# Kernel tuning notes

Hardware: AMD Instinct MI355X
Metric: run time of the kernel (lower is better)

## Reference

```python
import jax, jax.numpy as jnp
import numpy as np

B, T, D, H = 64, 512, 512, 1024


def setup_inputs() -> dict:
    key = jax.random.key(0)
    k_x, k_m, k_wi, k_wh = jax.random.split(key, 4)
    x = jax.random.normal(k_x, (B, T, D), dtype=jnp.float32)
    mask = jax.random.randint(k_m, (B, T), 0, 2, dtype=jnp.int32)
    # LSTMCell params: xavier_uniform for W_ih, orthogonal for W_hh, zero biases
    lim = float(np.sqrt(6.0 / (4 * H + D)))
    W_ih = jax.random.uniform(k_wi, (4 * H, D), dtype=jnp.float32, minval=-lim, maxval=lim)
    A = jax.random.normal(k_wh, (4 * H, H), dtype=jnp.float32)
    Q, _ = jnp.linalg.qr(A.T)  # (H, 4H) columns orthonormal -> rows of W_hh orthogonal-ish per torch init
    W_hh = Q.T.astype(jnp.float32)
    W_hh = jnp.concatenate([W_hh] * ((4 * H) // W_hh.shape[0]), axis=0)[: 4 * H]
    b_ih = jnp.zeros((4 * H,), dtype=jnp.float32)
    b_hh = jnp.zeros((4 * H,), dtype=jnp.float32)
    h0 = jnp.zeros((1, H), dtype=jnp.float32)
    c0 = jnp.zeros((1, H), dtype=jnp.float32)
    return {"x": x, "mask": mask, "W_ih": W_ih, "W_hh": W_hh,
            "b_ih": b_ih, "b_hh": b_hh, "h0": h0, "c0": c0}


def reference(x, mask, W_ih, W_hh, b_ih, b_hh, h0, c0):
    Bn, Tn, _ = x.shape
    Hn = h0.shape[1]
    # Precompute input projection for all timesteps: (B, T, 4H)
    xg = jnp.einsum('btd,gd->btg', x, W_ih) + b_ih + b_hh

    def step(carry, inp):
        h, c = carry
        xg_t, m_t = inp  # (B, 4H), (B,)
        gates = xg_t + h @ W_hh.T  # (B, 4H)
        i, f, g, o = jnp.split(gates, 4, axis=-1)  # torch LSTMCell gate order i,f,g,o
        i = jax.nn.sigmoid(i)
        f = jax.nn.sigmoid(f)
        g = jnp.tanh(g)
        o = jax.nn.sigmoid(o)
        c_new = f * c + i * g
        h_new = o * jnp.tanh(c_new)
        keep = (m_t != 0)[:, None]
        h2 = jnp.where(keep, h_new, h)
        c2 = jnp.where(keep, c_new, c)
        return (h2, c2), h2

    h_init = jnp.broadcast_to(h0, (Bn, Hn))
    c_init = jnp.broadcast_to(c0, (Bn, Hn))
    xs = (jnp.swapaxes(xg, 0, 1), mask.T)  # time-major for scan
    (_, _), hs = jax.lax.scan(step, (h_init, c_init), xs)
    return jnp.swapaxes(hs, 0, 1)  # (B, T, H)
```

## Files before the change

### kernel.cpp

```cpp
#include <hip/hip_runtime.h>

#define B_   64
#define T_   512
#define D_   512
#define H_   1024
#define G4   4096
#define KTOT 1536
#define KC_N 48
#define AP   1544

typedef float f32x4 __attribute__((ext_vector_type(4)));
typedef short s16x8 __attribute__((ext_vector_type(8)));

__device__ __forceinline__ unsigned short f2bf(float f) {
    unsigned int u = __float_as_uint(f);
    u = (u + 0x7fffu + ((u >> 16) & 1u)) >> 16;
    return (unsigned short)u;
}
__device__ __forceinline__ float bf2f(unsigned short h) {
    return __uint_as_float(((unsigned int)h) << 16);
}
__device__ __forceinline__ float sigm(float x) { return 1.f / (1.f + __expf(-x)); }
__device__ __forceinline__ float tanh_f(float x) { return 1.f - 2.f / (__expf(2.f * x) + 1.f); }

__global__ __launch_bounds__(256) void pack_w(const float* __restrict__ W_ih,
                                              const float* __restrict__ W_hh,
                                              unsigned short* __restrict__ Wpk) {
    int tid = blockIdx.x * 256 + threadIdx.x;
    int j    = tid & 7;
    int lane = (tid >> 3) & 63;
    int rest = tid >> 9;
    int kc = rest % KC_N;
    int c  = rest / KC_N;
    int npk = c * 16 + (lane & 15);
    int jh = npk >> 2, g = npk & 3;
    int row = g * H_ + jh;
    int k = kc * 32 + (lane >> 4) * 8 + j;
    float v = (k < D_) ? W_ih[row * D_ + k] : W_hh[row * H_ + (k - D_)];
    Wpk[tid] = f2bf(v);
}

__global__ __launch_bounds__(256) void init_state(const float* __restrict__ h0,
                                                  const float* __restrict__ c0,
                                                  const float* __restrict__ b_ih,
                                                  const float* __restrict__ b_hh,
                                                  unsigned short* __restrict__ h_a,
                                                  float* __restrict__ c_cur,
                                                  float* __restrict__ bias_p) {
    int tid = blockIdx.x * 256 + threadIdx.x;
    int j = tid & (H_ - 1);
    h_a[tid]  = f2bf(h0[j]);
    c_cur[tid] = c0[j];
    if (tid < G4) {
        int jh = tid >> 2, g = tid & 3;
        bias_p[tid] = b_ih[g * H_ + jh] + b_hh[g * H_ + jh];
    }
}

__global__ __launch_bounds__(256) void lstm_step(
    const float* __restrict__ x, const int* __restrict__ mask,
    const unsigned short* __restrict__ Wpk, const float* __restrict__ bias_p,
    const unsigned short* __restrict__ h_in, unsigned short* __restrict__ h_out,
    float* __restrict__ c_cur, float* __restrict__ out, int t)
{
    __shared__ unsigned short At[16 * AP];
    __shared__ float Dl[16][66];

    const int tid = threadIdx.x;
    const int b0 = blockIdx.y * 16;
    const int bx = blockIdx.x;

    #pragma unroll
    for (int i = 0; i < 8; ++i) {
        int e = i * 256 + tid;
        int r = e >> 7, c4 = e & 127;
        float4 v = *reinterpret_cast<const float4*>(x + ((b0 + r) * T_ + t) * D_ + c4 * 4);
        unsigned int lo = ((unsigned int)f2bf(v.y) << 16) | f2bf(v.x);
        unsigned int hi = ((unsigned int)f2bf(v.w) << 16) | f2bf(v.z);
        *reinterpret_cast<uint2*>(&At[r * AP + c4 * 4]) = make_uint2(lo, hi);
    }
    #pragma unroll
    for (int i = 0; i < 8; ++i) {
        int e = i * 256 + tid;
        int r = e >> 7, c8 = e & 127;
        uint4 v = *reinterpret_cast<const uint4*>(h_in + (b0 + r) * H_ + c8 * 8);
        *reinterpret_cast<uint4*>(&At[r * AP + D_ + c8 * 8]) = v;
    }
    __syncthreads();

    const int w = tid >> 6, l = tid & 63;
    const int quad = l >> 4, l15 = l & 15;
    const int cgrp = bx * 4 + w;

    f32x4 acc = {0.f, 0.f, 0.f, 0.f};
    const unsigned short* atp = &At[l15 * AP + quad * 8];
    const unsigned short* bp  = Wpk + ((size_t)(cgrp * KC_N) * 64 + l) * 8;
    #pragma unroll 4
    for (int kc = 0; kc < KC_N; ++kc) {
        s16x8 af = *reinterpret_cast<const s16x8*>(atp + kc * 32);
        s16x8 bf = *reinterpret_cast<const s16x8*>(bp + kc * 64 * 8);
        acc = __builtin_amdgcn_mfma_f32_16x16x32_bf16(af, bf, acc, 0, 0, 0);
    }
    #pragma unroll
    for (int r = 0; r < 4; ++r)
        Dl[quad * 4 + r][w * 16 + l15] = acc[r];
    __syncthreads();

    const int b = tid >> 4, u = tid & 15;
    const int jh = bx * 16 + u;
    float4 bias = *reinterpret_cast<const float4*>(bias_p + bx * 64 + u * 4);
    float gi = sigm (Dl[b][u * 4 + 0] + bias.x);
    float gf = sigm (Dl[b][u * 4 + 1] + bias.y);
    float gg = tanh_f(Dl[b][u * 4 + 2] + bias.z);
    float go = sigm (Dl[b][u * 4 + 3] + bias.w);

    const int sidx = (b0 + b) * H_ + jh;
    float c_old = c_cur[sidx];
    float h_old = bf2f(At[b * AP + D_ + jh]);
    float c_new = gf * c_old + gi * gg;
    float h_new = go * tanh_f(c_new);
    int m = mask[(b0 + b) * T_ + t];
    float h2 = m ? h_new : h_old;
    float c2 = m ? c_new : c_old;
    c_cur[sidx] = c2;
    h_out[sidx] = f2bf(h2);
    out[((size_t)(b0 + b) * T_ + t) * H_ + jh] = h2;
}

extern "C" void kernel_launch(void* const* d_in, const int* in_sizes, int n_in,
                              void* d_out, int out_size, void* d_ws, size_t ws_size,
                              hipStream_t stream)
{
    const float* x    = (const float*)d_in[0];
    const int*   mask = (const int*)d_in[1];
    const float* W_ih = (const float*)d_in[2];
    const float* W_hh = (const float*)d_in[3];
    const float* b_ih = (const float*)d_in[4];
    const float* b_hh = (const float*)d_in[5];
    const float* h0   = (const float*)d_in[6];
    const float* c0   = (const float*)d_in[7];
    float* out = (float*)d_out;

    char* wsb = (char*)d_ws;
    unsigned short* Wpk    = (unsigned short*)(wsb);
    float*          bias_p = (float*)(wsb + 12582912);
    unsigned short* h_a    = (unsigned short*)(wsb + 12599296);
    unsigned short* h_b    = (unsigned short*)(wsb + 12730368);
    float*          c_cur  = (float*)(wsb + 12861440);

    pack_w<<<24576, 256, 0, stream>>>(W_ih, W_hh, Wpk);
    init_state<<<256, 256, 0, stream>>>(h0, c0, b_ih, b_hh, h_a, c_cur, bias_p);

    dim3 grid(64, 4);
    for (int t = 0; t < T_; ++t) {
        const unsigned short* hin = (t & 1) ? h_b : h_a;
        unsigned short*      hout = (t & 1) ? h_a : h_b;
        lstm_step<<<grid, 256, 0, stream>>>(x, mask, Wpk, bias_p, hin, hout, c_cur, out, t);
    }
}
```

Before: 3.451 ms.

## Replace per-timestep launches with persistent LSTM kernel using grid barriers

```diff
diff --git a/kernel.cpp b/kernel.cpp
--- a/kernel.cpp
+++ b/kernel.cpp
@@ -5,9 +5,8 @@
 #define D_   512
 #define H_   1024
 #define G4   4096
-#define KTOT 1536
 #define KC_N 48
-#define AP   1544
+#define NBLK_HALF 128
 
 typedef float f32x4 __attribute__((ext_vector_type(4)));
 typedef short s16x8 __attribute__((ext_vector_type(8)));
@@ -17,11 +16,17 @@
     u = (u + 0x7fffu + ((u >> 16) & 1u)) >> 16;
     return (unsigned short)u;
 }
-__device__ __forceinline__ float bf2f(unsigned short h) {
-    return __uint_as_float(((unsigned int)h) << 16);
-}
 __device__ __forceinline__ float sigm(float x) { return 1.f / (1.f + __expf(-x)); }
 __device__ __forceinline__ float tanh_f(float x) { return 1.f - 2.f / (__expf(2.f * x) + 1.f); }
+
+__device__ __forceinline__ s16x8 cvt8(float4 a, float4 b) {
+    union { s16x8 v; unsigned int u[4]; } r;
+    asm("v_cvt_pk_bf16_f32 %0, %1, %2" : "=v"(r.u[0]) : "v"(a.x), "v"(a.y));
+    asm("v_cvt_pk_bf16_f32 %0, %1, %2" : "=v"(r.u[1]) : "v"(a.z), "v"(a.w));
+    asm("v_cvt_pk_bf16_f32 %0, %1, %2" : "=v"(r.u[2]) : "v"(b.x), "v"(b.y));
+    asm("v_cvt_pk_bf16_f32 %0, %1, %2" : "=v"(r.u[3]) : "v"(b.z), "v"(b.w));
+    return r.v;
+}
 
 __global__ __launch_bounds__(256) void pack_w(const float* __restrict__ W_ih,
                                               const float* __restrict__ W_hh,
@@ -40,91 +45,140 @@
     Wpk[tid] = f2bf(v);
 }
 
-__global__ __launch_bounds__(256) void init_state(const float* __restrict__ h0,
-                                                  const float* __restrict__ c0,
-                                                  const float* __restrict__ b_ih,
-                                                  const float* __restrict__ b_hh,
-                                                  unsigned short* __restrict__ h_a,
-                                                  float* __restrict__ c_cur,
-                                                  float* __restrict__ bias_p) {
+__global__ __launch_bounds__(256) void init_state2(
+    const float* __restrict__ h0, const float* __restrict__ b_ih,
+    const float* __restrict__ b_hh, unsigned short* __restrict__ hbuf,
+    float* __restrict__ bias_p, unsigned int* __restrict__ bar)
+{
     int tid = blockIdx.x * 256 + threadIdx.x;
     int j = tid & (H_ - 1);
-    h_a[tid]  = f2bf(h0[j]);
-    c_cur[tid] = c0[j];
+    hbuf[tid] = f2bf(h0[j]);
     if (tid < G4) {
         int jh = tid >> 2, g = tid & 3;
         bias_p[tid] = b_ih[g * H_ + jh] + b_hh[g * H_ + jh];
     }
-}
-
-__global__ __launch_bounds__(256) void lstm_step(
+    if (tid < 64) bar[tid] = 0u;
+}
+
+__global__ __launch_bounds__(512, 2) void lstm_persist(
     const float* __restrict__ x, const int* __restrict__ mask,
     const unsigned short* __restrict__ Wpk, const float* __restrict__ bias_p,
-    const unsigned short* __restrict__ h_in, unsigned short* __restrict__ h_out,
-    float* __restrict__ c_cur, float* __restrict__ out, int t)
+    const float* __restrict__ h0, const float* __restrict__ c0,
+    unsigned short* __restrict__ hbuf, float* __restrict__ out,
+    unsigned int* __restrict__ bar)
 {
-    __shared__ unsigned short At[16 * AP];
-    __shared__ float Dl[16][66];
-
     const int tid = threadIdx.x;
-    const int b0 = blockIdx.y * 16;
-    const int bx = blockIdx.x;
-
-    #pragma unroll
-    for (int i = 0; i < 8; ++i) {
-        int e = i * 256 + tid;
-        int r = e >> 7, c4 = e & 127;
-        float4 v = *reinterpret_cast<const float4*>(x + ((b0 + r) * T_ + t) * D_ + c4 * 4);
-        unsigned int lo = ((unsigned int)f2bf(v.y) << 16) | f2bf(v.x);
-        unsigned int hi = ((unsigned int)f2bf(v.w) << 16) | f2bf(v.z);
-        *reinterpret_cast<uint2*>(&At[r * AP + c4 * 4]) = make_uint2(lo, hi);
-    }
-    #pragma unroll
-    for (int i = 0; i < 8; ++i) {
-        int e = i * 256 + tid;
-        int r = e >> 7, c8 = e & 127;
-        uint4 v = *reinterpret_cast<const uint4*>(h_in + (b0 + r) * H_ + c8 * 8);
-        *reinterpret_cast<uint4*>(&At[r * AP + D_ + c8 * 8]) = v;
-    }
-    __syncthreads();
+    const int bid = blockIdx.x;
+    const int cg  = bid >> 1;
+    const int mh  = bid & 1;
+    const int b0g = mh << 5;
 
     const int w = tid >> 6, l = tid & 63;
     const int quad = l >> 4, l15 = l & 15;
-    const int cgrp = bx * 4 + w;
-
-    f32x4 acc = {0.f, 0.f, 0.f, 0.f};
-    const unsigned short* atp = &At[l15 * AP + quad * 8];
-    const unsigned short* bp  = Wpk + ((size_t)(cgrp * KC_N) * 64 + l) * 8;
-    #pragma unroll 4
-    for (int kc = 0; kc < KC_N; ++kc) {
-        s16x8 af = *reinterpret_cast<const s16x8*>(atp + kc * 32);
-        s16x8 bf = *reinterpret_cast<const s16x8*>(bp + kc * 64 * 8);
-        acc = __builtin_amdgcn_mfma_f32_16x16x32_bf16(af, bf, acc, 0, 0, 0);
-    }
+    const int mi = w >> 2;
+    const int ks = w & 3;
+    const int arow = b0g + mi * 16 + l15;
+
+    __shared__ float Dls[4][32][36];
+
+    s16x8 Bf0[12], Bf1[12];
     #pragma unroll
-    for (int r = 0; r < 4; ++r)
-        Dl[quad * 4 + r][w * 16 + l15] = acc[r];
-    __syncthreads();
-
-    const int b = tid >> 4, u = tid & 15;
-    const int jh = bx * 16 + u;
-    float4 bias = *reinterpret_cast<const float4*>(bias_p + bx * 64 + u * 4);
-    float gi = sigm (Dl[b][u * 4 + 0] + bias.x);
-    float gf = sigm (Dl[b][u * 4 + 1] + bias.y);
-    float gg = tanh_f(Dl[b][u * 4 + 2] + bias.z);
-    float go = sigm (Dl[b][u * 4 + 3] + bias.w);
-
-    const int sidx = (b0 + b) * H_ + jh;
-    float c_old = c_cur[sidx];
-    float h_old = bf2f(At[b * AP + D_ + jh]);
-    float c_new = gf * c_old + gi * gg;
-    float h_new = go * tanh_f(c_new);
-    int m = mask[(b0 + b) * T_ + t];
-    float h2 = m ? h_new : h_old;
-    float c2 = m ? c_new : c_old;
-    c_cur[sidx] = c2;
-    h_out[sidx] = f2bf(h2);
-    out[((size_t)(b0 + b) * T_ + t) * H_ + jh] = h2;
+    for (int i = 0; i < 12; ++i) {
+        int kc = ks * 12 + i;
+        Bf0[i] = *reinterpret_cast<const s16x8*>(Wpk + (size_t)(((cg * 2 + 0) * KC_N + kc) * 64 + l) * 8);
+        Bf1[i] = *reinterpret_cast<const s16x8*>(Wpk + (size_t)(((cg * 2 + 1) * KC_N + kc) * 64 + l) * 8);
+    }
+
+    const int b_l = tid >> 3, u = tid & 7;
+    const int brow = b0g + b_l;
+    const int jcol = cg * 8 + u;
+    float c_reg = 0.f, h_reg = 0.f;
+    float4 bias = make_float4(0.f, 0.f, 0.f, 0.f);
+    if (tid < 256) {
+        c_reg = c0[jcol];
+        h_reg = h0[jcol];
+        bias = *reinterpret_cast<const float4*>(bias_p + cg * 32 + u * 4);
+    }
+
+    unsigned int* cnt = bar + mh * 32;
+
+    #pragma unroll 1
+    for (int t = 0; t < T_; ++t) {
+        const unsigned short* hin  = hbuf + (size_t)(t & 1) * (B_ * H_);
+        unsigned short*       hout = hbuf + (size_t)((t + 1) & 1) * (B_ * H_);
+
+        f32x4 a0 = {0.f, 0.f, 0.f, 0.f}, a1 = {0.f, 0.f, 0.f, 0.f};
+        const float* xrow = x + ((size_t)arow * T_ + t) * D_;
+        #pragma unroll
+        for (int i = 0; i < 12; ++i) {
+            int kc = ks * 12 + i;
+            s16x8 af;
+            if (kc < 16) {
+                const float* xp = xrow + kc * 32 + quad * 8;
+                float4 v0 = *reinterpret_cast<const float4*>(xp);
+                float4 v1 = *reinterpret_cast<const float4*>(xp + 4);
+                af = cvt8(v0, v1);
+            } else {
+                const unsigned int* hp = reinterpret_cast<const unsigned int*>(
+                    hin + (size_t)arow * H_ + (kc - 16) * 32 + quad * 8);
+                union { s16x8 v; unsigned int u4[4]; } au;
+                au.u4[0] = __hip_atomic_load(hp + 0, __ATOMIC_RELAXED, __HIP_MEMORY_SCOPE_AGENT);
+                au.u4[1] = __hip_atomic_load(hp + 1, __ATOMIC_RELAXED, __HIP_MEMORY_SCOPE_AGENT);
+                au.u4[2] = __hip_atomic_load(hp + 2, __ATOMIC_RELAXED, __HIP_MEMORY_SCOPE_AGENT);
+                au.u4[3] = __hip_atomic_load(hp + 3, __ATOMIC_RELAXED, __HIP_MEMORY_SCOPE_AGENT);
+                af = au.v;
+            }
+            a0 = __builtin_amdgcn_mfma_f32_16x16x32_bf16(af, Bf0[i], a0, 0, 0, 0);
+            a1 = __builtin_amdgcn_mfma_f32_16x16x32_bf16(af, Bf1[i], a1, 0, 0, 0);
+        }
+        #pragma unroll
+        for (int r = 0; r < 4; ++r) {
+            Dls[ks][mi * 16 + quad * 4 + r][l15]      = a0[r];
+            Dls[ks][mi * 16 + quad * 4 + r][16 + l15] = a1[r];
+        }
+        __syncthreads();
+
+        if (tid < 256) {
+            f32x4 s0 = *reinterpret_cast<f32x4*>(&Dls[0][b_l][u * 4]);
+            f32x4 s1 = *reinterpret_cast<f32x4*>(&Dls[1][b_l][u * 4]);
+            f32x4 s2 = *reinterpret_cast<f32x4*>(&Dls[2][b_l][u * 4]);
+            f32x4 s3 = *reinterpret_cast<f32x4*>(&Dls[3][b_l][u * 4]);
+            f32x4 g = s0 + s1 + s2 + s3;
+            float gi = sigm  (g[0] + bias.x);
+            float gf = sigm  (g[1] + bias.y);
+            float gg = tanh_f(g[2] + bias.z);
+            float go = sigm  (g[3] + bias.w);
+            float c_new = gf * c_reg + gi * gg;
+            float h_new = go * tanh_f(c_new);
+            int m = mask[(size_t)brow * T_ + t];
+            float h2 = m ? h_new : h_reg;
+            c_reg = m ? c_new : c_reg;
+            h_reg = h2;
+            out[((size_t)brow * T_ + t) * H_ + jcol] = h2;
+            unsigned int hv = (unsigned int)f2bf(h2);
+            unsigned int hx = (unsigned int)__shfl_xor((int)hv, 1);
+            if ((u & 1) == 0) {
+                unsigned int pk = (hx << 16) | hv;
+                __hip_atomic_store(reinterpret_cast<unsigned int*>(hout + (size_t)brow * H_ + jcol),
+                                   pk, __ATOMIC_RELAXED, __HIP_MEMORY_SCOPE_AGENT);
+            }
+        }
+        __syncthreads();
+
+        if (t < T_ - 1) {
+            if (tid == 0) {
+                __hip_atomic_fetch_add(cnt, 1u, __ATOMIC_RELAXED, __HIP_MEMORY_SCOPE_AGENT);
+                const unsigned int target = (unsigned int)(t + 1) * NBLK_HALF;
+                int guard = 0;
+                while (__hip_atomic_load(cnt, __ATOMIC_RELAXED, __HIP_MEMORY_SCOPE_AGENT) < target) {
+                    __builtin_amdgcn_s_sleep(2);
+                    if (++guard > (1 << 20)) break;
+                }
+            }
+            __builtin_amdgcn_fence(__ATOMIC_ACQUIRE, "workgroup");
+            __syncthreads();
+        }
+    }
 }
 
 extern "C" void kernel_launch(void* const* d_in, const int* in_sizes, int n_in,
@@ -144,17 +198,10 @@
     char* wsb = (char*)d_ws;
     unsigned short* Wpk    = (unsigned short*)(wsb);
     float*          bias_p = (float*)(wsb + 12582912);
-    unsigned short* h_a    = (unsigned short*)(wsb + 12599296);
-    unsigned short* h_b    = (unsigned short*)(wsb + 12730368);
-    float*          c_cur  = (float*)(wsb + 12861440);
+    unsigned short* hbuf   = (unsigned short*)(wsb + 12599296);
+    unsigned int*   bar    = (unsigned int*)(wsb + 12861440);
 
     pack_w<<<24576, 256, 0, stream>>>(W_ih, W_hh, Wpk);
-    init_state<<<256, 256, 0, stream>>>(h0, c0, b_ih, b_hh, h_a, c_cur, bias_p);
-
-    dim3 grid(64, 4);
-    for (int t = 0; t < T_; ++t) {
-        const unsigned short* hin = (t & 1) ? h_b : h_a;
-        unsigned short*      hout = (t & 1) ? h_a : h_b;
-        lstm_step<<<grid, 256, 0, stream>>>(x, mask, Wpk, bias_p, hin, hout, c_cur, out, t);
-    }
-}
+    init_state2<<<256, 256, 0, stream>>>(h0, b_ih, b_hh, hbuf, bias_p, bar);
+    lstm_persist<<<256, 512, 0, stream>>>(x, mask, Wpk, bias_p, h0, c0, hbuf, out, bar);
+}
```

Result: slower. 6.507 ms (+88.5%).

## Split K across waves with 32x32 register tiles and direct global A loads

Applied to the files above, without the earlier changes.

```diff
diff --git a/kernel.cpp b/kernel.cpp
--- a/kernel.cpp
+++ b/kernel.cpp
@@ -5,9 +5,7 @@
 #define D_   512
 #define H_   1024
 #define G4   4096
-#define KTOT 1536
 #define KC_N 48
-#define AP   1544
 
 typedef float f32x4 __attribute__((ext_vector_type(4)));
 typedef short s16x8 __attribute__((ext_vector_type(8)));
@@ -22,6 +20,15 @@
 }
 __device__ __forceinline__ float sigm(float x) { return 1.f / (1.f + __expf(-x)); }
 __device__ __forceinline__ float tanh_f(float x) { return 1.f - 2.f / (__expf(2.f * x) + 1.f); }
+
+__device__ __forceinline__ s16x8 cvt8(float4 a, float4 b) {
+    union { s16x8 v; unsigned int u[4]; } r;
+    asm("v_cvt_pk_bf16_f32 %0, %1, %2" : "=v"(r.u[0]) : "v"(a.x), "v"(a.y));
+    asm("v_cvt_pk_bf16_f32 %0, %1, %2" : "=v"(r.u[1]) : "v"(a.z), "v"(a.w));
+    asm("v_cvt_pk_bf16_f32 %0, %1, %2" : "=v"(r.u[2]) : "v"(b.x), "v"(b.y));
+    asm("v_cvt_pk_bf16_f32 %0, %1, %2" : "=v"(r.u[3]) : "v"(b.z), "v"(b.w));
+    return r.v;
+}
 
 __global__ __launch_bounds__(256) void pack_w(const float* __restrict__ W_ih,
                                               const float* __restrict__ W_hh,
@@ -57,74 +64,92 @@
     }
 }
 
-__global__ __launch_bounds__(256) void lstm_step(
+__global__ __launch_bounds__(512) void lstm_step2(
     const float* __restrict__ x, const int* __restrict__ mask,
     const unsigned short* __restrict__ Wpk, const float* __restrict__ bias_p,
     const unsigned short* __restrict__ h_in, unsigned short* __restrict__ h_out,
     float* __restrict__ c_cur, float* __restrict__ out, int t)
 {
-    __shared__ unsigned short At[16 * AP];
-    __shared__ float Dl[16][66];
+    const int tid = threadIdx.x;
+    const int cg  = blockIdx.x;
+    const int mh  = blockIdx.y;
+    const int b0g = mh << 5;
 
-    const int tid = threadIdx.x;
-    const int b0 = blockIdx.y * 16;
-    const int bx = blockIdx.x;
+    const int w = tid >> 6, l = tid & 63;
+    const int quad = l >> 4, l15 = l & 15;
+
+    __shared__ float Dls[8][32][36];
+
+    const int b_l = tid >> 3, u = tid & 7;
+    const int brow = b0g + b_l;
+    const int jcol = cg * 8 + u;
+
+    int mv = 0; float c_old = 0.f, h_old = 0.f;
+    if (tid < 256) {
+        mv    = mask[(size_t)brow * T_ + t];
+        c_old = c_cur[(size_t)brow * H_ + jcol];
+        h_old = bf2f(h_in[(size_t)brow * H_ + jcol]);
+    }
+
+    f32x4 acc00 = {0,0,0,0}, acc01 = {0,0,0,0}, acc10 = {0,0,0,0}, acc11 = {0,0,0,0};
+    const unsigned short* bp0 = Wpk + (((size_t)(cg * 2 + 0) * KC_N) * 64 + l) * 8;
+    const unsigned short* bp1 = Wpk + (((size_t)(cg * 2 + 1) * KC_N) * 64 + l) * 8;
+    const int r0 = b0g + l15;
+    const int r1 = b0g + 16 + l15;
 
     #pragma unroll
-    for (int i = 0; i < 8; ++i) {
-        int e = i * 256 + tid;
-        int r = e >> 7, c4 = e & 127;
-        float4 v = *reinterpret_cast<const float4*>(x + ((b0 + r) * T_ + t) * D_ + c4 * 4);
-        unsigned int lo = ((unsigned int)f2bf(v.y) << 16) | f2bf(v.x);
-        unsigned int hi = ((unsigned int)f2bf(v.w) << 16) | f2bf(v.z);
-        *reinterpret_cast<uint2*>(&At[r * AP + c4 * 4]) = make_uint2(lo, hi);
+    for (int i = 0; i < 6; ++i) {
+        const int kc = w * 6 + i;
+        s16x8 b0 = *reinterpret_cast<const s16x8*>(bp0 + (size_t)kc * 512);
+        s16x8 b1 = *reinterpret_cast<const s16x8*>(bp1 + (size_t)kc * 512);
+        s16x8 a0, a1;
+        if (kc < 16) {
+            const float* xp0 = x + ((size_t)r0 * T_ + t) * D_ + kc * 32 + quad * 8;
+            const float* xp1 = x + ((size_t)r1 * T_ + t) * D_ + kc * 32 + quad * 8;
+            float4 v0 = *reinterpret_cast<const float4*>(xp0);
+            float4 v1 = *reinterpret_cast<const float4*>(xp0 + 4);
+            float4 v2 = *reinterpret_cast<const float4*>(xp1);
+            float4 v3 = *reinterpret_cast<const float4*>(xp1 + 4);
+            a0 = cvt8(v0, v1);
+            a1 = cvt8(v2, v3);
+        } else {
+            const int hk = (kc - 16) * 32 + quad * 8;
+            a0 = *reinterpret_cast<const s16x8*>(h_in + (size_t)r0 * H_ + hk);
+            a1 = *reinterpret_cast<const s16x8*>(h_in + (size_t)r1 * H_ + hk);
+        }
+        acc00 = __builtin_amdgcn_mfma_f32_16x16x32_bf16(a0, b0, acc00, 0, 0, 0);
+        acc01 = __builtin_amdgcn_mfma_f32_16x16x32_bf16(a0, b1, acc01, 0, 0, 0);
+        acc10 = __builtin_amdgcn_mfma_f32_16x16x32_bf16(a1, b0, acc10, 0, 0, 0);
+        acc11 = __builtin_amdgcn_mfma_f32_16x16x32_bf16(a1, b1, acc11, 0, 0, 0);
     }
     #pragma unroll
-    for (int i = 0; i < 8; ++i) {
-        int e = i * 256 + tid;
-        int r = e >> 7, c8 = e & 127;
-        uint4 v = *reinterpret_cast<const uint4*>(h_in + (b0 + r) * H_ + c8 * 8);
-        *reinterpret_cast<uint4*>(&At[r * AP + D_ + c8 * 8]) = v;
+    for (int r = 0; r < 4; ++r) {
+        Dls[w][quad * 4 + r][l15]           = acc00[r];
+        Dls[w][quad * 4 + r][16 + l15]      = acc01[r];
+        Dls[w][16 + quad * 4 + r][l15]      = acc10[r];
+        Dls[w][16 + quad * 4 + r][16 + l15] = acc11[r];
     }
     __syncthreads();
 
-    const int w = tid >> 6, l = tid & 63;
-    const int quad = l >> 4, l15 = l & 15;
-    const int cgrp = bx * 4 + w;
-
-    f32x4 acc = {0.f, 0.f, 0.f, 0.f};
-    const unsigned short* atp = &At[l15 * AP + quad * 8];
-    const unsigned short* bp  = Wpk + ((size_t)(cgrp * KC_N) * 64 + l) * 8;
-    #pragma unroll 4
-    for (int kc = 0; kc < KC_N; ++kc) {
-        s16x8 af = *reinterpret_cast<const s16x8*>(atp + kc * 32);
-        s16x8 bf = *reinterpret_cast<const s16x8*>(bp + kc * 64 * 8);
-        acc = __builtin_amdgcn_mfma_f32_16x16x32_bf16(af, bf, acc, 0, 0, 0);
+    if (tid < 256) {
+        f32x4 g = (f32x4){0,0,0,0};
+        #pragma unroll
+        for (int ww = 0; ww < 8; ++ww)
+            g += *reinterpret_cast<f32x4*>(&Dls[ww][b_l][u * 4]);
+        float4 bias = *reinterpret_cast<const float4*>(bias_p + cg * 32 + u * 4);
+        float gi = sigm  (g[0] + bias.x);
+        float gf = sigm  (g[1] + bias.y);
+        float gg = tanh_f(g[2] + bias.z);
+        float go = sigm  (g[3] + bias.w);
+        float c_new = gf * c_old + gi * gg;
+        float h_new = go * tanh_f(c_new);
+        float h2 = mv ? h_new : h_old;
+        float c2 = mv ? c_new : c_old;
+        const size_t sidx = (size_t)brow * H_ + jcol;
+        c_cur[sidx] = c2;
+        h_out[sidx] = f2bf(h2);
+        out[((size_t)brow * T_ + t) * H_ + jcol] = h2;
     }
-    #pragma unroll
-    for (int r = 0; r < 4; ++r)
-        Dl[quad * 4 + r][w * 16 + l15] = acc[r];
-    __syncthreads();
-
-    const int b = tid >> 4, u = tid & 15;
-    const int jh = bx * 16 + u;
-    float4 bias = *reinterpret_cast<const float4*>(bias_p + bx * 64 + u * 4);
-    float gi = sigm (Dl[b][u * 4 + 0] + bias.x);
-    float gf = sigm (Dl[b][u * 4 + 1] + bias.y);
-    float gg = tanh_f(Dl[b][u * 4 + 2] + bias.z);
-    float go = sigm (Dl[b][u * 4 + 3] + bias.w);
-
-    const int sidx = (b0 + b) * H_ + jh;
-    float c_old = c_cur[sidx];
-    float h_old = bf2f(At[b * AP + D_ + jh]);
-    float c_new = gf * c_old + gi * gg;
-    float h_new = go * tanh_f(c_new);
-    int m = mask[(b0 + b) * T_ + t];
-    float h2 = m ? h_new : h_old;
-    float c2 = m ? c_new : c_old;
-    c_cur[sidx] = c2;
-    h_out[sidx] = f2bf(h2);
-    out[((size_t)(b0 + b) * T_ + t) * H_ + jh] = h2;
 }
 
 extern "C" void kernel_launch(void* const* d_in, const int* in_sizes, int n_in,
@@ -151,10 +176,10 @@
     pack_w<<<24576, 256, 0, stream>>>(W_ih, W_hh, Wpk);
     init_state<<<256, 256, 0, stream>>>(h0, c0, b_ih, b_hh, h_a, c_cur, bias_p);
 
-    dim3 grid(64, 4);
+    dim3 grid(128, 2);
     for (int t = 0; t < T_; ++t) {
         const unsigned short* hin = (t & 1) ? h_b : h_a;
         unsigned short*      hout = (t & 1) ? h_a : h_b;
-        lstm_step<<<grid, 256, 0, stream>>>(x, mask, Wpk, bias_p, hin, hout, c_cur, out, t);
+        lstm_step2<<<grid, 512, 0, stream>>>(x, mask, Wpk, bias_p, hin, hout, c_cur, out, t);
     }
 }
```

After: 4.715 ms. 36.6% more time.
